# Performance work log

Measured on AMD Instinct MI355X. Metric: run time of the kernel, lower is better.

Reference implementation:

```python
import jax, jax.numpy as jnp
import numpy as np

N_NODES = 100000
N_EDGES = 1600000
N_GRAPHS = 64
F = 50
N_LAYERS = 3
EPS_STD = 1e-5
EPS_BN = 1e-5


def _glorot(key, shape):
    fan_in, fan_out = shape[0], shape[1]
    lim = float(np.sqrt(6.0 / (fan_in + fan_out)))
    return jax.random.uniform(key, shape, jnp.float32, -lim, lim)


def setup_inputs() -> dict:
    key = jax.random.key(0)
    ks = jax.random.split(key, 20)
    x = jax.random.normal(ks[0], (N_NODES, 2), jnp.float32)
    edge_index = jax.random.randint(ks[1], (2, N_EDGES), 0, N_NODES, jnp.int32)
    batch_ids = jnp.sort(jax.random.randint(ks[2], (N_NODES,), 0, N_GRAPHS, jnp.int32))
    inp = {
        "x": x,
        "edge_index": edge_index,
        "batch_ids": batch_ids,
        "W_gcn": _glorot(ks[3], (2, F)),
        "b_gcn": jnp.zeros((F,), jnp.float32),
        # stacked per-layer PNA params [L, ...]
        "pre_W": jnp.stack([_glorot(jax.random.fold_in(ks[4], i), (2 * F, F)) for i in range(N_LAYERS)]),
        "pre_b": jnp.zeros((N_LAYERS, F), jnp.float32),
        "post_W": jnp.stack([_glorot(jax.random.fold_in(ks[5], i), (13 * F, F)) for i in range(N_LAYERS)]),
        "post_b": jnp.zeros((N_LAYERS, F), jnp.float32),
        "lin_W": jnp.stack([_glorot(jax.random.fold_in(ks[6], i), (F, F)) for i in range(N_LAYERS)]),
        "lin_b": jnp.zeros((N_LAYERS, F), jnp.float32),
        "bn_gamma": jnp.ones((N_LAYERS, F), jnp.float32),
        "bn_beta": jnp.zeros((N_LAYERS, F), jnp.float32),
        "mlp_W1": _glorot(ks[7], (F, 25)),
        "mlp_b1": jnp.zeros((25,), jnp.float32),
        "mlp_W2": _glorot(ks[8], (25, 1)),
        "mlp_b2": jnp.zeros((1,), jnp.float32),
    }
    return inp


def _pna_layer(x, src, dst, deg_raw, deg_c, avg_log, Wp, bp, Wq, bq, Wl, bl):
    # pre-NN on messages: concat(x_i, x_j) -> F   (i = target/dst, j = source/src)
    h = jnp.concatenate([x[dst], x[src]], axis=-1) @ Wp + bp  # [E, F]
    dc = deg_c[:, None]
    s = jax.ops.segment_sum(h, dst, num_segments=N_NODES)
    mean = s / dc
    mean_sq = jax.ops.segment_sum(h * h, dst, num_segments=N_NODES) / dc
    var = jax.nn.relu(mean_sq - mean * mean)
    std = jnp.sqrt(var + EPS_STD)
    has_edge = (deg_raw > 0)[:, None]
    mn = jnp.where(has_edge, jax.ops.segment_min(h, dst, num_segments=N_NODES), 0.0)
    mx = jnp.where(has_edge, jax.ops.segment_max(h, dst, num_segments=N_NODES), 0.0)
    agg = jnp.concatenate([mean, mn, mx, std], axis=-1)  # [N, 4F]
    amp = (jnp.log1p(deg_c) / avg_log)[:, None]
    att = (avg_log / jnp.log1p(deg_c))[:, None]
    out = jnp.concatenate([agg, agg * amp, agg * att], axis=-1)  # [N, 12F]
    out = jnp.concatenate([x, out], axis=-1) @ Wq + bq  # post-NN: [N, 13F] -> F
    return out @ Wl + bl


def reference(x, edge_index, batch_ids, W_gcn, b_gcn, pre_W, pre_b, post_W, post_b,
              lin_W, lin_b, bn_gamma, bn_beta, mlp_W1, mlp_b1, mlp_W2, mlp_b2):
    src, dst = edge_index[0], edge_index[1]

    # ---- GCNConv(2 -> 50) with self loops + symmetric normalization ----
    h = x @ W_gcn
    loop = jnp.arange(N_NODES, dtype=src.dtype)
    src_a = jnp.concatenate([src, loop])
    dst_a = jnp.concatenate([dst, loop])
    deg_sl = jax.ops.segment_sum(jnp.ones_like(src_a, jnp.float32), dst_a, num_segments=N_NODES)
    dinv = jnp.where(deg_sl > 0, jax.lax.rsqrt(deg_sl), 0.0)
    norm = (dinv[src_a] * dinv[dst_a])[:, None]
    h = jax.ops.segment_sum(h[src_a] * norm, dst_a, num_segments=N_NODES) + b_gcn

    # ---- degree stats for PNA scalers ----
    deg_raw = jax.ops.segment_sum(jnp.ones_like(src, jnp.float32), dst, num_segments=N_NODES)
    deg_c = jnp.maximum(deg_raw, 1.0)
    avg_log = jnp.mean(jnp.log1p(deg_raw))

    for l in range(N_LAYERS):
        h = _pna_layer(h, src, dst, deg_raw, deg_c, avg_log,
                       pre_W[l], pre_b[l], post_W[l], post_b[l], lin_W[l], lin_b[l])
        mu = jnp.mean(h, axis=0)
        var = jnp.mean((h - mu) ** 2, axis=0)
        h = (h - mu) * jax.lax.rsqrt(var + EPS_BN) * bn_gamma[l] + bn_beta[l]
        h = jax.nn.relu(h)

    # ---- global add pool + MLP (dropout is identity at eval) ----
    g = jax.ops.segment_sum(h, batch_ids, num_segments=N_GRAPHS)  # [G, F]
    g = jax.nn.relu(g @ mlp_W1 + mlp_b1)
    g = g @ mlp_W2 + mlp_b2  # [G, 1]
    return g.reshape(N_GRAPHS)
```

## Files before the change

kernel.cpp:

```cpp
#include <hip/hip_runtime.h>
#include <math.h>

#define NN 100000
#define NE 1600000
#define NG 64
#define FF 50
#define NL 3
#define NBUCK ((NN + 255) / 256)

typedef short bf16x8 __attribute__((ext_vector_type(8)));
typedef float f32x4 __attribute__((ext_vector_type(4)));

__device__ __forceinline__ short f2bf(float f) {
  return __builtin_bit_cast(short, (__bf16)f);
}
__device__ __forceinline__ float bf2f(short s) {
  unsigned int u = ((unsigned int)(unsigned short)s) << 16;
  return __builtin_bit_cast(float, u);
}
__device__ __forceinline__ float2 unpk2(unsigned u) {
  float2 v;
  v.x = __builtin_bit_cast(float, u << 16);
  v.y = __builtin_bit_cast(float, u & 0xFFFF0000u);
  return v;
}
__device__ __forceinline__ unsigned pk2(float2 v) {
  return (unsigned)(unsigned short)f2bf(v.x) | ((unsigned)(unsigned short)f2bf(v.y) << 16);
}

__device__ __forceinline__ bf16x8 ldfrag_bn(const short* base, const float2* __restrict__ ab, int kbase) {
  bf16x8 raw = *(const bf16x8*)base;
  unsigned u[4];
  __builtin_memcpy(u, &raw, 16);
  short t[8] __attribute__((aligned(16)));
#pragma unroll
  for (int i = 0; i < 4; ++i) {
    float2 v = unpk2(u[i]);
    float2 a0 = ab[kbase + 2 * i], a1 = ab[kbase + 2 * i + 1];
    v.x = fmaxf(fmaf(v.x, a0.x, a0.y), 0.f);
    v.y = fmaxf(fmaf(v.y, a1.x, a1.y), 0.f);
    ((unsigned*)t)[i] = pk2(v);
  }
  bf16x8 r;
  __builtin_memcpy(&r, t, 16);
  return r;
}

__global__ void k_deg(const int* __restrict__ dst, int* __restrict__ deg) {
  int e = blockIdx.x * blockDim.x + threadIdx.x;
  if (e < NE) atomicAdd(&deg[dst[e]], 1);
}

__global__ void k_scan1(const int* __restrict__ deg, int* __restrict__ off, int* __restrict__ parts) {
  __shared__ int sm[1024];
  int i = blockIdx.x * 1024 + threadIdx.x;
  int v = (i < NN) ? deg[i] : 0;
  sm[threadIdx.x] = v;
  __syncthreads();
  for (int ofs = 1; ofs < 1024; ofs <<= 1) {
    int t = (threadIdx.x >= ofs) ? sm[threadIdx.x - ofs] : 0;
    __syncthreads();
    sm[threadIdx.x] += t;
    __syncthreads();
  }
  if (i < NN) off[i] = sm[threadIdx.x] - v;
  if (threadIdx.x == 1023) parts[blockIdx.x] = sm[1023];
}

__global__ void k_scan2(int* __restrict__ parts, int nb) {
  __shared__ int sm[128];
  int v = (threadIdx.x < nb) ? parts[threadIdx.x] : 0;
  sm[threadIdx.x] = v;
  __syncthreads();
  for (int ofs = 1; ofs < 128; ofs <<= 1) {
    int t = (threadIdx.x >= ofs) ? sm[threadIdx.x - ofs] : 0;
    __syncthreads();
    sm[threadIdx.x] += t;
    __syncthreads();
  }
  if (threadIdx.x < nb) parts[threadIdx.x] = sm[threadIdx.x] - v;
}

__global__ void k_scan3(int* __restrict__ off, const int* __restrict__ parts, int* __restrict__ bcur) {
  int i = blockIdx.x * 256 + threadIdx.x;
  if (i < NN) {
    int v = off[i] + parts[i >> 10];
    off[i] = v;
    if ((i & 255) == 0) bcur[i >> 8] = v;
  }
  if (i == 0) off[NN] = NE;
}

__global__ void k_nodeinit(const int* __restrict__ deg, float* __restrict__ dinv,
                           float* __restrict__ lgc, float* __restrict__ scal) {
  int i = blockIdx.x * 256 + threadIdx.x;
  float lp = 0.f;
  if (i < NN) {
    int d = deg[i];
    dinv[i] = rsqrtf((float)(d + 1));
    int dc = d > 1 ? d : 1;
    lgc[i] = log1pf((float)dc);
    lp = log1pf((float)d);
  }
  for (int o = 32; o > 0; o >>= 1) lp += __shfl_down(lp, o);
  __shared__ float red[4];
  int lane = threadIdx.x & 63, w = threadIdx.x >> 6;
  if (lane == 0) red[w] = lp;
  __syncthreads();
  if (threadIdx.x == 0) atomicAdd(scal, red[0] + red[1] + red[2] + red[3]);
}

__global__ __launch_bounds__(256) void k_bucket(const int* __restrict__ src, const int* __restrict__ dst,
                                                int* __restrict__ bcur, unsigned* __restrict__ tmp) {
  __shared__ int hist[NBUCK];
  __shared__ int base[NBUCK];
  int t = threadIdx.x;
  for (int i = t; i < NBUCK; i += 256) hist[i] = 0;
  __syncthreads();
  int e0 = blockIdx.x * 4096;
  int myb[16], myrank[16];
  unsigned mypack[16];
#pragma unroll
  for (int i = 0; i < 16; ++i) {
    int e = e0 + i * 256 + t;
    if (e < NE) {
      int s = src[e], d = dst[e];
      int b = d >> 8;
      myb[i] = b;
      mypack[i] = ((unsigned)(d & 255) << 17) | (unsigned)s;
      myrank[i] = atomicAdd(&hist[b], 1);
    } else myb[i] = -1;
  }
  __syncthreads();
  for (int i = t; i < NBUCK; i += 256)
    base[i] = hist[i] ? atomicAdd(&bcur[i], hist[i]) : 0;
  __syncthreads();
#pragma unroll
  for (int i = 0; i < 16; ++i)
    if (myb[i] >= 0) tmp[base[myb[i]] + myrank[i]] = mypack[i];
}

__global__ __launch_bounds__(256) void k_bsort(const int* __restrict__ off, const unsigned* __restrict__ tmp,
                                               int* __restrict__ ssrc) {
  int b = blockIdx.x;
  int n0 = b * 256;
  int nEnd = n0 + 256 < NN ? n0 + 256 : NN;
  __shared__ int cnt[256];
  __shared__ int nb[256];
  int t = threadIdx.x;
  cnt[t] = 0;
  if (n0 + t < nEnd) nb[t] = off[n0 + t];
  __syncthreads();
  int lo = off[n0], hiE = off[nEnd];
  for (int e = lo + t; e < hiE; e += 256) {
    unsigned p = tmp[e];
    int dloc = p >> 17;
    int s = (int)(p & 0x1FFFFu);
    int pos = nb[dloc] + atomicAdd(&cnt[dloc], 1);
    ssrc[pos] = s;
  }
}

__global__ void k_fusew(const float* __restrict__ postW, const float* __restrict__ postb,
                        const float* __restrict__ linW, const float* __restrict__ linb,
                        float* __restrict__ A, float* __restrict__ bias2) {
  int wid = (blockIdx.x * blockDim.x + threadIdx.x) >> 6;
  int f = threadIdx.x & 63;
  if (wid >= 3 * 651) return;
  int l = wid / 651, r = wid % 651;
  int fc = f < FF ? f : FF - 1;
  const float* lw = linW + l * FF * FF;
  float acc = 0.f;
  if (r < 650) {
    const float* pw = postW + (l * 650 + r) * FF;
    for (int j = 0; j < FF; ++j) acc += pw[j] * lw[j * FF + fc];
    if (f < FF) A[(l * 650 + r) * FF + f] = acc;
  } else {
    const float* pb = postb + l * FF;
    for (int j = 0; j < FF; ++j) acc += pb[j] * lw[j * FF + fc];
    bias2[l * 64 + f] = (f < FF) ? (acc + linb[l * FF + f]) : 0.f;
  }
}

__global__ void k_packA(const float* __restrict__ Af, short* __restrict__ Abt) {
  int t = blockIdx.x * 256 + threadIdx.x;
  if (t >= 3 * 13 * 64 * 64) return;
  int kk = t & 63;
  int f = (t >> 6) & 63;
  int lc = t >> 12;
  int c = lc % 13;
  int l = lc / 13;
  float v = 0.f;
  if (kk < FF && f < FF) v = Af[((size_t)(l * 650 + c * FF + kk)) * FF + f];
  Abt[t] = f2bf(v);
}

__global__ void k_packP(const float* __restrict__ preW, short* __restrict__ Pbt) {
  int t = blockIdx.x * 256 + threadIdx.x;
  if (t >= NL * 2 * 64 * 64) return;
  int kk = t & 63;
  int f = (t >> 6) & 63;
  int ls = t >> 12;
  int s = ls & 1, l = ls >> 1;
  float v = 0.f;
  if (kk < FF && f < FF) v = preW[(size_t)(l * 100 + s * FF + kk) * FF + f];
  Pbt[t] = f2bf(v);
}

__global__ void k_gcnpre(const float* __restrict__ x, const float* __restrict__ Wg,
                         const float* __restrict__ dinv, short* __restrict__ pb) {
  int t = blockIdx.x * 256 + threadIdx.x;
  int n = t >> 6, f = t & 63;
  if (n >= NN) return;
  float v = 0.f;
  if (f < FF) v = (x[2 * n] * Wg[f] + x[2 * n + 1] * Wg[FF + f]) * dinv[n];
  pb[n * 64 + f] = f2bf(v);
}

__global__ void k_gcnagg(const short* __restrict__ pb, const int* __restrict__ off,
                         const int* __restrict__ ssrc, const float* __restrict__ dinv,
                         const float* __restrict__ bg, short* __restrict__ hb) {
  int wid = (blockIdx.x * blockDim.x + threadIdx.x) >> 6;
  int lane = threadIdx.x & 63;
  if (wid >= NN) return;
  int n = wid;
  int p = lane & 31;
  int hf = lane >> 5;
  float2 acc;
  {
    float2 sv = unpk2(*(const unsigned*)(pb + n * 64 + 2 * p));
    acc.x = hf ? 0.f : sv.x;
    acc.y = hf ? 0.f : sv.y;
  }
  int lo = off[n], hi = off[n + 1];
  for (int base = lo; base < hi; base += 64) {
    int rem = hi - base;
    int cnt = rem > 64 ? 64 : rem;
    int sidx = (base + lane < hi) ? ssrc[base + lane] : 0;
    int pairs = cnt >> 1;
    int j = 0;
    for (; j + 4 <= pairs; j += 4) {
#pragma unroll
      for (int i = 0; i < 4; ++i) {
        int s = __shfl(sidx, 2 * (j + i) + hf);
        float2 v = unpk2(*(const unsigned*)(pb + s * 64 + 2 * p));
        acc.x += v.x; acc.y += v.y;
      }
    }
    for (; j < pairs; ++j) {
      int s = __shfl(sidx, 2 * j + hf);
      float2 v = unpk2(*(const unsigned*)(pb + s * 64 + 2 * p));
      acc.x += v.x; acc.y += v.y;
    }
    if (cnt & 1) {
      int s = __shfl(sidx, cnt - 1);
      float2 v = unpk2(*(const unsigned*)(pb + s * 64 + 2 * p));
      if (hf == 0) { acc.x += v.x; acc.y += v.y; }
    }
  }
  acc.x += __shfl_xor(acc.x, 32);
  acc.y += __shfl_xor(acc.y, 32);
  if (lane < 32) {
    float2 o = make_float2(0.f, 0.f);
    if (p < 25) {
      float dv = dinv[n];
      float2 bgp = *(const float2*)(bg + 2 * p);
      o = make_float2(dv * acc.x + bgp.x, dv * acc.y + bgp.y);
    }
    ((unsigned*)(hb + n * 64))[p] = pk2(o);
  }
}

__global__ __launch_bounds__(256) void k_preM(const short* __restrict__ hin, const float2* __restrict__ ab,
                                              const short* __restrict__ Pbt, const float* __restrict__ preb,
                                              short* __restrict__ cbh, short* __restrict__ bbh, int l) {
  int tid = threadIdx.x;
  int w = tid >> 6, lane = tid & 63;
  int q = lane >> 4, m16 = lane & 15;
  int n0 = blockIdx.x * 64 + w * 16;
  int anode = n0 + m16;
  int nsafe = anode < NN ? anode : 0;
  bf16x8 afr[2];
#pragma unroll
  for (int hh = 0; hh < 2; ++hh) {
    const short* srcp = hin + (size_t)nsafe * 64 + hh * 32 + q * 8;
    afr[hh] = ab ? ldfrag_bn(srcp, ab, hh * 32 + q * 8) : *(const bf16x8*)srcp;
  }
  const short* P0 = Pbt + l * 8192;
  f32x4 aT[4], aB2[4];
#pragma unroll
  for (int ft = 0; ft < 4; ++ft) {
    aT[ft] = (f32x4){0.f, 0.f, 0.f, 0.f};
    aB2[ft] = (f32x4){0.f, 0.f, 0.f, 0.f};
  }
#pragma unroll
  for (int hh = 0; hh < 2; ++hh) {
#pragma unroll
    for (int ft = 0; ft < 4; ++ft) {
      bf16x8 b0 = *(const bf16x8*)(P0 + ((ft * 16 + m16) << 6) + hh * 32 + q * 8);
      bf16x8 b1 = *(const bf16x8*)(P0 + 4096 + ((ft * 16 + m16) << 6) + hh * 32 + q * 8);
      aT[ft] = __builtin_amdgcn_mfma_f32_16x16x32_bf16(afr[hh], b0, aT[ft], 0, 0, 0);
      aB2[ft] = __builtin_amdgcn_mfma_f32_16x16x32_bf16(afr[hh], b1, aB2[ft], 0, 0, 0);
    }
  }
#pragma unroll
  for (int r = 0; r < 4; ++r) {
    int node = n0 + q * 4 + r;
    if (node >= NN) continue;
#pragma unroll
    for (int ft = 0; ft < 4; ++ft) {
      int col = ft * 16 + m16;
      cbh[node * 64 + col] = (col < FF) ? f2bf(aT[ft][r] + preb[l * FF + col]) : 0;
      bbh[node * 64 + col] = f2bf(aB2[ft][r]);
    }
  }
}

__global__ void k_agg(const short* __restrict__ bbh, const short* __restrict__ cbh,
                      const int* __restrict__ off, const int* __restrict__ ssrc,
                      const float* __restrict__ lgc, const float* __restrict__ scal,
                      short* __restrict__ agb, float* __restrict__ ampatt) {
  int wid = (blockIdx.x * blockDim.x + threadIdx.x) >> 6;
  int lane = threadIdx.x & 63;
  if (wid >= NN) return;
  int n = wid;
  int p = lane & 31;
  int hf = lane >> 5;
  float2 S = {0.f, 0.f}, S2 = {0.f, 0.f};
  float2 MN = {INFINITY, INFINITY}, MX = {-INFINITY, -INFINITY};
  int lo = off[n], hi = off[n + 1];
  for (int base = lo; base < hi; base += 64) {
    int rem = hi - base;
    int cnt = rem > 64 ? 64 : rem;
    int sidx = (base + lane < hi) ? ssrc[base + lane] : 0;
    int pairs = cnt >> 1;
    int j = 0;
    for (; j + 4 <= pairs; j += 4) {
#pragma unroll
      for (int i = 0; i < 4; ++i) {
        int s = __shfl(sidx, 2 * (j + i) + hf);
        float2 v = unpk2(*(const unsigned*)(bbh + s * 64 + 2 * p));
        S.x += v.x; S.y += v.y;
        S2.x = fmaf(v.x, v.x, S2.x); S2.y = fmaf(v.y, v.y, S2.y);
        MN.x = fminf(MN.x, v.x); MN.y = fminf(MN.y, v.y);
        MX.x = fmaxf(MX.x, v.x); MX.y = fmaxf(MX.y, v.y);
      }
    }
    for (; j < pairs; ++j) {
      int s = __shfl(sidx, 2 * j + hf);
      float2 v = unpk2(*(const unsigned*)(bbh + s * 64 + 2 * p));
      S.x += v.x; S.y += v.y;
      S2.x = fmaf(v.x, v.x, S2.x); S2.y = fmaf(v.y, v.y, S2.y);
      MN.x = fminf(MN.x, v.x); MN.y = fminf(MN.y, v.y);
      MX.x = fmaxf(MX.x, v.x); MX.y = fmaxf(MX.y, v.y);
    }
    if (cnt & 1) {
      int s = __shfl(sidx, cnt - 1);
      float2 v = unpk2(*(const unsigned*)(bbh + s * 64 + 2 * p));
      if (hf == 0) {
        S.x += v.x; S.y += v.y;
        S2.x = fmaf(v.x, v.x, S2.x); S2.y = fmaf(v.y, v.y, S2.y);
        MN.x = fminf(MN.x, v.x); MN.y = fminf(MN.y, v.y);
        MX.x = fmaxf(MX.x, v.x); MX.y = fmaxf(MX.y, v.y);
      }
    }
  }
  S.x += __shfl_xor(S.x, 32);   S.y += __shfl_xor(S.y, 32);
  S2.x += __shfl_xor(S2.x, 32); S2.y += __shfl_xor(S2.y, 32);
  MN.x = fminf(MN.x, __shfl_xor(MN.x, 32)); MN.y = fminf(MN.y, __shfl_xor(MN.y, 32));
  MX.x = fmaxf(MX.x, __shfl_xor(MX.x, 32)); MX.y = fmaxf(MX.y, __shfl_xor(MX.y, 32));
  int d = hi - lo;
  bool valid = p < 25;
  float2 mean, mnv, mxv, stdv;
  if (d > 0) {
    float inv = 1.f / (float)d;
    float2 m = make_float2(S.x * inv, S.y * inv);
    float vx = S2.x * inv - m.x * m.x; vx = vx > 0.f ? vx : 0.f;
    float vy = S2.y * inv - m.y * m.y; vy = vy > 0.f ? vy : 0.f;
    stdv = make_float2(sqrtf(vx + 1e-5f), sqrtf(vy + 1e-5f));
    float2 c = valid ? unpk2(((const unsigned*)(cbh + n * 64))[p]) : make_float2(0.f, 0.f);
    mean = make_float2(c.x + m.x, c.y + m.y);
    mnv = make_float2(c.x + MN.x, c.y + MN.y);
    mxv = make_float2(c.x + MX.x, c.y + MX.y);
  } else {
    mean = mnv = mxv = make_float2(0.f, 0.f);
    float sq = sqrtf(1e-5f);
    stdv = make_float2(sq, sq);
  }
  if (lane < 32) {
    unsigned* row32 = (unsigned*)(agb + (size_t)n * 256);
    row32[p]      = valid ? pk2(mean) : 0u;
    row32[32 + p] = valid ? pk2(mnv) : 0u;
    row32[64 + p] = valid ? pk2(mxv) : 0u;
    row32[96 + p] = valid ? pk2(stdv) : 0u;
  }
  if (lane == 0) {
    float avg = scal[0] * (1.f / NN);
    float lg = lgc[n];
    ampatt[2 * n] = lg / avg;
    ampatt[2 * n + 1] = avg / lg;
  }
}

__global__ __launch_bounds__(512, 2) void k_gemm(const short* __restrict__ h, const float2* __restrict__ ab,
                                                 const short* __restrict__ agb, const float* __restrict__ ampatt,
                                                 const short* __restrict__ Abt, const float* __restrict__ bias2,
                                                 short* __restrict__ hout, float* __restrict__ bnsumR) {
  __shared__ short Bs[3][64][72];
  int tid = threadIdx.x;
  int w = tid >> 6, lane = tid & 63;
  int q = lane >> 4, m16 = lane & 15;
  int n0 = blockIdx.x * 128 + w * 16;

  int anode = n0 + m16;
  int nsafe = anode < NN ? anode : 0;
  bf16x8 afr[5][2];
  {
#pragma unroll
    for (int hh = 0; hh < 2; ++hh) {
      const short* srcp = h + (size_t)nsafe * 64 + hh * 32 + q * 8;
      afr[0][hh] = ab ? ldfrag_bn(srcp, ab, hh * 32 + q * 8) : *(const bf16x8*)srcp;
    }
    const short* arow = agb + (size_t)nsafe * 256;
#pragma unroll
    for (int c = 1; c <= 4; ++c)
#pragma unroll
      for (int hh = 0; hh < 2; ++hh)
        afr[c][hh] = *(const bf16x8*)(arow + (c - 1) * 64 + hh * 32 + q * 8);
  }

  f32x4 acc[3][4];
#pragma unroll
  for (int s = 0; s < 3; ++s)
#pragma unroll
    for (int ft = 0; ft < 4; ++ft) acc[s][ft] = (f32x4){0.f, 0.f, 0.f, 0.f};

  bool stager = tid < 256;
  int bf = tid >> 2;
  int bko = (tid & 3) * 16;
  float4 rg[3][2];
  if (stager) {
    const float4* g = (const float4*)(Abt + (bf << 6) + bko);
    rg[0][0] = g[0]; rg[0][1] = g[1];
  }
  for (int ph = 0; ph < 5; ++ph) {
    int nslice = (ph == 0) ? 1 : 3;
    if (ph) __syncthreads();
    if (stager) {
      for (int s = 0; s < nslice; ++s) {
        *(float4*)&Bs[s][bf][bko] = rg[s][0];
        *(float4*)&Bs[s][bf][bko + 8] = rg[s][1];
      }
    }
    __syncthreads();
    if (stager && ph < 4) {
#pragma unroll
      for (int s = 0; s < 3; ++s) {
        int chunk = (ph + 1) + 4 * s;
        const float4* g = (const float4*)(Abt + (chunk << 12) + (bf << 6) + bko);
        rg[s][0] = g[0]; rg[s][1] = g[1];
      }
    }
    if (ph == 0) {
#pragma unroll
      for (int hh = 0; hh < 2; ++hh)
#pragma unroll
        for (int ft = 0; ft < 4; ++ft) {
          bf16x8 b = *(const bf16x8*)&Bs[0][ft * 16 + m16][hh * 32 + q * 8];
          acc[0][ft] = __builtin_amdgcn_mfma_f32_16x16x32_bf16(afr[0][hh], b, acc[0][ft], 0, 0, 0);
        }
    } else {
#pragma unroll
      for (int hh = 0; hh < 2; ++hh)
#pragma unroll
        for (int s = 0; s < 3; ++s)
#pragma unroll
          for (int ft = 0; ft < 4; ++ft) {
            bf16x8 b = *(const bf16x8*)&Bs[s][ft * 16 + m16][hh * 32 + q * 8];
            acc[s][ft] = __builtin_amdgcn_mfma_f32_16x16x32_bf16(afr[ph][hh], b, acc[s][ft], 0, 0, 0);
          }
    }
  }

  float sacc[4] = {0.f, 0.f, 0.f, 0.f};
  float qacc[4] = {0.f, 0.f, 0.f, 0.f};
#pragma unroll
  for (int r = 0; r < 4; ++r) {
    int node = n0 + q * 4 + r;
    if (node >= NN) continue;
    float2 aa = *(const float2*)(ampatt + 2 * node);
#pragma unroll
    for (int ft = 0; ft < 4; ++ft) {
      int col = ft * 16 + m16;
      float val = 0.f;
      if (col < FF) {
        val = acc[0][ft][r] + aa.x * acc[1][ft][r] + aa.y * acc[2][ft][r] + bias2[col];
        sacc[ft] += val;
        qacc[ft] = fmaf(val, val, qacc[ft]);
      }
      hout[node * 64 + col] = f2bf(val);
    }
  }
#pragma unroll
  for (int ft = 0; ft < 4; ++ft) {
    sacc[ft] += __shfl_xor(sacc[ft], 16);
    sacc[ft] += __shfl_xor(sacc[ft], 32);
    qacc[ft] += __shfl_xor(qacc[ft], 16);
    qacc[ft] += __shfl_xor(qacc[ft], 32);
  }
  __syncthreads();
  float* red = (float*)&Bs[0][0][0];
  if (lane < 16) {
#pragma unroll
    for (int ft = 0; ft < 4; ++ft) {
      red[w * 128 + ft * 16 + lane]      = sacc[ft];
      red[w * 128 + 64 + ft * 16 + lane] = qacc[ft];
    }
  }
  __syncthreads();
  if (tid < 128) {
    float v = 0.f;
#pragma unroll
    for (int i = 0; i < 8; ++i) v += red[i * 128 + tid];
    atomicAdd(&bnsumR[(blockIdx.x & 7) * 128 + tid], v);
  }
}

__global__ void k_bnab(const float* __restrict__ bnsumR, const float* __restrict__ gamma,
                       const float* __restrict__ beta, float2* __restrict__ ab, int l) {
  int f = threadIdx.x;
  float a = 0.f, b = 0.f;
  if (f < FF) {
    float s = 0.f, q = 0.f;
    for (int r = 0; r < 8; ++r) { s += bnsumR[r * 128 + f]; q += bnsumR[r * 128 + 64 + f]; }
    float mu = s * (1.f / NN);
    float vq = q * (1.f / NN) - mu * mu;
    float rs = rsqrtf((vq > 0.f ? vq : 0.f) + 1e-5f);
    a = rs * gamma[l * FF + f];
    b = beta[l * FF + f] - mu * a;
  }
  ab[f] = make_float2(a, b);
}

__global__ void k_gsum(const short* __restrict__ h, const float2* __restrict__ ab,
                       const int* __restrict__ batch, float* __restrict__ gsum) {
  int w = threadIdx.x >> 6, lane = threadIdx.x & 63;
  int fc = lane < FF ? lane : FF - 1;
  bool act = lane < FF;
  float2 p = ab[fc];
  int n0 = blockIdx.x * 256 + w * 64;
  if (n0 >= NN) return;
  int nEnd = n0 + 64 < NN ? n0 + 64 : NN;
  float acc = 0.f;
  int gcur = batch[n0];
  for (int n = n0; n < nEnd; ++n) {
    int g = batch[n];
    if (g != gcur) {
      if (act) atomicAdd(&gsum[gcur * 64 + lane], acc);
      acc = 0.f; gcur = g;
    }
    float v = bf2f(h[n * 64 + fc]);
    acc += fmaxf(fmaf(v, p.x, p.y), 0.f);
  }
  if (act) atomicAdd(&gsum[gcur * 64 + lane], acc);
}

__global__ void k_mlp(const float* __restrict__ gsum, const float* __restrict__ W1,
                      const float* __restrict__ b1, const float* __restrict__ W2,
                      const float* __restrict__ b2, float* __restrict__ out) {
  int g = threadIdx.x;
  if (g >= NG) return;
  float gv[FF];
#pragma unroll
  for (int f = 0; f < FF; ++f) gv[f] = gsum[g * 64 + f];
  float r = b2[0];
  for (int j = 0; j < 25; ++j) {
    float a = b1[j];
#pragma unroll
    for (int f = 0; f < FF; ++f) a = fmaf(gv[f], W1[f * 25 + j], a);
    r += fmaxf(a, 0.f) * W2[j];
  }
  out[g] = r;
}

extern "C" void kernel_launch(void* const* d_in, const int* in_sizes, int n_in,
                              void* d_out, int out_size, void* d_ws, size_t ws_size,
                              hipStream_t stream) {
  const float* x     = (const float*)d_in[0];
  const int*   ei    = (const int*)d_in[1];
  const int*   src   = ei;
  const int*   dst   = ei + NE;
  const int*   batch = (const int*)d_in[2];
  const float* Wg    = (const float*)d_in[3];
  const float* bg    = (const float*)d_in[4];
  const float* preW  = (const float*)d_in[5];
  const float* preb  = (const float*)d_in[6];
  const float* postW = (const float*)d_in[7];
  const float* postb = (const float*)d_in[8];
  const float* linW  = (const float*)d_in[9];
  const float* linb  = (const float*)d_in[10];
  const float* gamma = (const float*)d_in[11];
  const float* beta  = (const float*)d_in[12];
  const float* W1    = (const float*)d_in[13];
  const float* b1    = (const float*)d_in[14];
  const float* W2    = (const float*)d_in[15];
  const float* b2    = (const float*)d_in[16];
  float* out = (float*)d_out;

  char* W = (char*)d_ws;
  int*    deg    = (int*)(W + 0);
  int*    off    = (int*)(W + 400384);
  int*    bcur   = (int*)(W + 801280);
  int*    parts  = (int*)(W + 803328);
  float*  dinv   = (float*)(W + 807424);
  float*  lgc    = (float*)(W + 1207808);
  float*  scal   = (float*)(W + 1608192);
  float*  bnsum  = (float*)(W + 1608704);
  float2* ab     = (float2*)(W + 1620992);
  float*  Af     = (float*)(W + 1622528);
  float*  bias2  = (float*)(W + 2012672);
  short*  Abt    = (short*)(W + 2013696);
  short*  Pbt    = (short*)(W + 2333184);
  unsigned* tmp  = (unsigned*)(W + 2382336);
  int*    ssrc   = (int*)(W + 8782336);
  short*  hA     = (short*)(W + 15182336);
  short*  hB     = (short*)(W + 27982592);
  short*  cbh    = (short*)(W + 40782848);
  short*  bbh    = (short*)(W + 53583104);
  short*  agb    = (short*)(W + 66383360);
  float*  ampatt = (float*)(W + 117583616);
  float*  gsum   = (float*)(W + 118383872);

  hipMemsetAsync(deg, 0, 400384, stream);
  hipMemsetAsync(scal, 0, 12800, stream);
  hipMemsetAsync(gsum, 0, 16384, stream);

  k_deg<<<(NE + 255) / 256, 256, 0, stream>>>(dst, deg);
  k_scan1<<<98, 1024, 0, stream>>>(deg, off, parts);
  k_scan2<<<1, 128, 0, stream>>>(parts, 98);
  k_scan3<<<(NN + 255) / 256, 256, 0, stream>>>(off, parts, bcur);
  k_nodeinit<<<(NN + 255) / 256, 256, 0, stream>>>(deg, dinv, lgc, scal);
  k_bucket<<<(NE + 4095) / 4096, 256, 0, stream>>>(src, dst, bcur, tmp);
  k_bsort<<<NBUCK, 256, 0, stream>>>(off, tmp, ssrc);
  k_fusew<<<(3 * 651 + 3) / 4, 256, 0, stream>>>(postW, postb, linW, linb, Af, bias2);
  k_packA<<<(3 * 13 * 64 * 64 + 255) / 256, 256, 0, stream>>>(Af, Abt);
  k_packP<<<(NL * 2 * 64 * 64 + 255) / 256, 256, 0, stream>>>(preW, Pbt);

  k_gcnpre<<<NN / 4, 256, 0, stream>>>(x, Wg, dinv, bbh);
  k_gcnagg<<<NN / 4, 256, 0, stream>>>(bbh, off, ssrc, dinv, bg, hA);

  short* hin = hA;
  short* hout = hB;
  for (int l = 0; l < NL; ++l) {
    const float2* abl = (l == 0) ? nullptr : (ab + (l - 1) * 64);
    k_preM<<<(NN + 63) / 64, 256, 0, stream>>>(hin, abl, Pbt, preb, cbh, bbh, l);
    k_agg<<<NN / 4, 256, 0, stream>>>(bbh, cbh, off, ssrc, lgc, scal, agb, ampatt);
    k_gemm<<<(NN + 127) / 128, 512, 0, stream>>>(hin, abl, agb, ampatt,
                                                 Abt + l * 13 * 4096, bias2 + l * 64, hout,
                                                 bnsum + l * 1024);
    k_bnab<<<1, 64, 0, stream>>>(bnsum + l * 1024, gamma, beta, ab + l * 64, l);
    short* t = hin; hin = hout; hout = t;
  }
  k_gsum<<<NBUCK, 256, 0, stream>>>(hin, ab + 2 * 64, batch, gsum);
  k_mlp<<<1, 64, 0, stream>>>(gsum, W1, b1, W2, b2, out);
}
```

Measured before the change: 726.9 us.

## Fuse CSR construction into fixed-capacity bucketing and in-block degree counting

```diff
diff --git a/kernel.cpp b/kernel.cpp
--- a/kernel.cpp
+++ b/kernel.cpp
@@ -7,6 +7,7 @@
 #define FF 50
 #define NL 3
 #define NBUCK ((NN + 255) / 256)
+#define CAP 8192
 
 typedef short bf16x8 __attribute__((ext_vector_type(8)));
 typedef float f32x4 __attribute__((ext_vector_type(4)));
@@ -46,72 +47,8 @@
   return r;
 }
 
-__global__ void k_deg(const int* __restrict__ dst, int* __restrict__ deg) {
-  int e = blockIdx.x * blockDim.x + threadIdx.x;
-  if (e < NE) atomicAdd(&deg[dst[e]], 1);
-}
-
-__global__ void k_scan1(const int* __restrict__ deg, int* __restrict__ off, int* __restrict__ parts) {
-  __shared__ int sm[1024];
-  int i = blockIdx.x * 1024 + threadIdx.x;
-  int v = (i < NN) ? deg[i] : 0;
-  sm[threadIdx.x] = v;
-  __syncthreads();
-  for (int ofs = 1; ofs < 1024; ofs <<= 1) {
-    int t = (threadIdx.x >= ofs) ? sm[threadIdx.x - ofs] : 0;
-    __syncthreads();
-    sm[threadIdx.x] += t;
-    __syncthreads();
-  }
-  if (i < NN) off[i] = sm[threadIdx.x] - v;
-  if (threadIdx.x == 1023) parts[blockIdx.x] = sm[1023];
-}
-
-__global__ void k_scan2(int* __restrict__ parts, int nb) {
-  __shared__ int sm[128];
-  int v = (threadIdx.x < nb) ? parts[threadIdx.x] : 0;
-  sm[threadIdx.x] = v;
-  __syncthreads();
-  for (int ofs = 1; ofs < 128; ofs <<= 1) {
-    int t = (threadIdx.x >= ofs) ? sm[threadIdx.x - ofs] : 0;
-    __syncthreads();
-    sm[threadIdx.x] += t;
-    __syncthreads();
-  }
-  if (threadIdx.x < nb) parts[threadIdx.x] = sm[threadIdx.x] - v;
-}
-
-__global__ void k_scan3(int* __restrict__ off, const int* __restrict__ parts, int* __restrict__ bcur) {
-  int i = blockIdx.x * 256 + threadIdx.x;
-  if (i < NN) {
-    int v = off[i] + parts[i >> 10];
-    off[i] = v;
-    if ((i & 255) == 0) bcur[i >> 8] = v;
-  }
-  if (i == 0) off[NN] = NE;
-}
-
-__global__ void k_nodeinit(const int* __restrict__ deg, float* __restrict__ dinv,
-                           float* __restrict__ lgc, float* __restrict__ scal) {
-  int i = blockIdx.x * 256 + threadIdx.x;
-  float lp = 0.f;
-  if (i < NN) {
-    int d = deg[i];
-    dinv[i] = rsqrtf((float)(d + 1));
-    int dc = d > 1 ? d : 1;
-    lgc[i] = log1pf((float)dc);
-    lp = log1pf((float)d);
-  }
-  for (int o = 32; o > 0; o >>= 1) lp += __shfl_down(lp, o);
-  __shared__ float red[4];
-  int lane = threadIdx.x & 63, w = threadIdx.x >> 6;
-  if (lane == 0) red[w] = lp;
-  __syncthreads();
-  if (threadIdx.x == 0) atomicAdd(scal, red[0] + red[1] + red[2] + red[3]);
-}
-
-__global__ __launch_bounds__(256) void k_bucket(const int* __restrict__ src, const int* __restrict__ dst,
-                                                int* __restrict__ bcur, unsigned* __restrict__ tmp) {
+__global__ __launch_bounds__(256) void k_bucket2(const int* __restrict__ src, const int* __restrict__ dst,
+                                                 int* __restrict__ bcnt, unsigned* __restrict__ tmp) {
   __shared__ int hist[NBUCK];
   __shared__ int base[NBUCK];
   int t = threadIdx.x;
@@ -133,31 +70,84 @@
   }
   __syncthreads();
   for (int i = t; i < NBUCK; i += 256)
-    base[i] = hist[i] ? atomicAdd(&bcur[i], hist[i]) : 0;
+    base[i] = hist[i] ? atomicAdd(&bcnt[i], hist[i]) : 0;
   __syncthreads();
 #pragma unroll
   for (int i = 0; i < 16; ++i)
-    if (myb[i] >= 0) tmp[base[myb[i]] + myrank[i]] = mypack[i];
-}
-
-__global__ __launch_bounds__(256) void k_bsort(const int* __restrict__ off, const unsigned* __restrict__ tmp,
-                                               int* __restrict__ ssrc) {
-  int b = blockIdx.x;
-  int n0 = b * 256;
-  int nEnd = n0 + 256 < NN ? n0 + 256 : NN;
-  __shared__ int cnt[256];
-  __shared__ int nb[256];
+    if (myb[i] >= 0) {
+      int pos = base[myb[i]] + myrank[i];
+      if (pos < CAP) tmp[(size_t)myb[i] * CAP + pos] = mypack[i];
+    }
+}
+
+__global__ void k_bscan(const int* __restrict__ bcnt, int* __restrict__ bbase, int* __restrict__ off) {
+  __shared__ int sm[512];
   int t = threadIdx.x;
-  cnt[t] = 0;
-  if (n0 + t < nEnd) nb[t] = off[n0 + t];
-  __syncthreads();
-  int lo = off[n0], hiE = off[nEnd];
-  for (int e = lo + t; e < hiE; e += 256) {
-    unsigned p = tmp[e];
-    int dloc = p >> 17;
-    int s = (int)(p & 0x1FFFFu);
-    int pos = nb[dloc] + atomicAdd(&cnt[dloc], 1);
-    ssrc[pos] = s;
+  int v = (t < NBUCK) ? bcnt[t] : 0;
+  sm[t] = v;
+  __syncthreads();
+  for (int o = 1; o < 512; o <<= 1) {
+    int u = (t >= o) ? sm[t - o] : 0;
+    __syncthreads();
+    sm[t] += u;
+    __syncthreads();
+  }
+  if (t < NBUCK) bbase[t] = sm[t] - v;
+  if (t == 0) off[NN] = NE;
+}
+
+__global__ __launch_bounds__(256) void k_bsort2(const unsigned* __restrict__ tmp, const int* __restrict__ bcnt,
+                                                const int* __restrict__ bbase, int* __restrict__ off,
+                                                int* __restrict__ ssrc, float* __restrict__ dinv,
+                                                float* __restrict__ lgc, float* __restrict__ scal) {
+  __shared__ unsigned seg[CAP];
+  __shared__ int loc[256];
+  __shared__ int wred[4];
+  __shared__ float fred[4];
+  int b = blockIdx.x, t = threadIdx.x;
+  int c = bcnt[b];
+  if (c > CAP) c = CAP;
+  int base = bbase[b];
+  const unsigned* sp = tmp + (size_t)b * CAP;
+  loc[t] = 0;
+  __syncthreads();
+  for (int e = t; e < c; e += 256) {
+    unsigned p = sp[e];
+    seg[e] = p;
+    atomicAdd(&loc[p >> 17], 1);
+  }
+  __syncthreads();
+  int d = loc[t];
+  int lane = t & 63, w = t >> 6;
+  int v = d;
+#pragma unroll
+  for (int o = 1; o < 64; o <<= 1) {
+    int u = __shfl_up(v, o);
+    if (lane >= o) v += u;
+  }
+  if (lane == 63) wred[w] = v;
+  int n = b * 256 + t;
+  float lp = (n < NN) ? log1pf((float)d) : 0.f;
+#pragma unroll
+  for (int o = 32; o > 0; o >>= 1) lp += __shfl_down(lp, o);
+  if (lane == 0) fred[w] = lp;
+  __syncthreads();
+  int excl = v - d;
+#pragma unroll
+  for (int i = 0; i < 4; ++i)
+    if (i < w) excl += wred[i];
+  if (t == 0) atomicAdd(scal, fred[0] + fred[1] + fred[2] + fred[3]);
+  if (n < NN) {
+    off[n] = base + excl;
+    dinv[n] = rsqrtf((float)(d + 1));
+    lgc[n] = log1pf((float)(d > 1 ? d : 1));
+  }
+  loc[t] = base + excl;
+  __syncthreads();
+  for (int e = t; e < c; e += 256) {
+    unsigned p = seg[e];
+    int pos = atomicAdd(&loc[p >> 17], 1);
+    ssrc[pos] = (int)(p & 0x1FFFFu);
   }
 }
 
@@ -608,10 +598,9 @@
   float* out = (float*)d_out;
 
   char* W = (char*)d_ws;
-  int*    deg    = (int*)(W + 0);
+  int*    bcnt   = (int*)(W + 0);
+  int*    bbase  = (int*)(W + 2048);
   int*    off    = (int*)(W + 400384);
-  int*    bcur   = (int*)(W + 801280);
-  int*    parts  = (int*)(W + 803328);
   float*  dinv   = (float*)(W + 807424);
   float*  lgc    = (float*)(W + 1207808);
   float*  scal   = (float*)(W + 1608192);
@@ -621,7 +610,6 @@
   float*  bias2  = (float*)(W + 2012672);
   short*  Abt    = (short*)(W + 2013696);
   short*  Pbt    = (short*)(W + 2333184);
-  unsigned* tmp  = (unsigned*)(W + 2382336);
   int*    ssrc   = (int*)(W + 8782336);
   short*  hA     = (short*)(W + 15182336);
   short*  hB     = (short*)(W + 27982592);
@@ -630,18 +618,15 @@
   short*  agb    = (short*)(W + 66383360);
   float*  ampatt = (float*)(W + 117583616);
   float*  gsum   = (float*)(W + 118383872);
-
-  hipMemsetAsync(deg, 0, 400384, stream);
+  unsigned* tmp  = (unsigned*)agb;
+
+  hipMemsetAsync(bcnt, 0, 2048, stream);
   hipMemsetAsync(scal, 0, 12800, stream);
   hipMemsetAsync(gsum, 0, 16384, stream);
 
-  k_deg<<<(NE + 255) / 256, 256, 0, stream>>>(dst, deg);
-  k_scan1<<<98, 1024, 0, stream>>>(deg, off, parts);
-  k_scan2<<<1, 128, 0, stream>>>(parts, 98);
-  k_scan3<<<(NN + 255) / 256, 256, 0, stream>>>(off, parts, bcur);
-  k_nodeinit<<<(NN + 255) / 256, 256, 0, stream>>>(deg, dinv, lgc, scal);
-  k_bucket<<<(NE + 4095) / 4096, 256, 0, stream>>>(src, dst, bcur, tmp);
-  k_bsort<<<NBUCK, 256, 0, stream>>>(off, tmp, ssrc);
+  k_bucket2<<<(NE + 4095) / 4096, 256, 0, stream>>>(src, dst, bcnt, tmp);
+  k_bscan<<<1, 512, 0, stream>>>(bcnt, bbase, off);
+  k_bsort2<<<NBUCK, 256, 0, stream>>>(tmp, bcnt, bbase, off, ssrc, dinv, lgc, scal);
   k_fusew<<<(3 * 651 + 3) / 4, 256, 0, stream>>>(postW, postb, linW, linb, Af, bias2);
   k_packA<<<(3 * 13 * 64 * 64 + 255) / 256, 256, 0, stream>>>(Af, Abt);
   k_packP<<<(NL * 2 * 64 * 64 + 255) / 256, 256, 0, stream>>>(preW, Pbt);
```

New measurement: 659.4 us. 9.3% less time.
